# Performance work log

Measured on AMD Instinct MI355X. Metric: run time of the kernel, lower is better.

## Reference

```python
import jax, jax.numpy as jnp
import numpy as np

B, N, F, H, F_ = 2048, 8192, 512, 8, 64

def setup_inputs() -> dict:
    key = jax.random.key(0)
    k1, k2, k3, k4 = jax.random.split(key, 4)
    X = jax.random.normal(k1, (B, F), dtype=jnp.float32)
    G = jax.random.normal(k2, (N, F), dtype=jnp.float32)
    W = jax.random.normal(k3, (H, F, F_), dtype=jnp.float32) * 0.05   # per-head kernels
    att = jax.random.normal(k4, (H, 2 * F_), dtype=jnp.float32) * 0.05  # per-head att kernels (2F_,1) flattened
    return {"X": X, "G": G, "W": W, "att": att}

def reference(X, G, W, att):
    f_ = W.shape[-1]
    # Per-head linear transforms
    WhX = jnp.einsum('bf,hfe->hbe', X, W)   # [H,B,F_]
    WhG = jnp.einsum('nf,hfe->hne', G, W)   # [H,N,F_]
    # concat([WhX_i, WhG_j]) @ a  ==  WhX_i @ a1 + WhG_j @ a2  -> avoids tiled [B*N,2F_]
    a1, a2 = att[:, :f_], att[:, f_:]
    e1 = jnp.einsum('hbe,he->hb', WhX, a1)  # [H,B]
    e2 = jnp.einsum('hne,he->hn', WhG, a2)  # [H,N]
    scores = e1[:, :, None] + e2[:, None, :]            # [H,B,N] pairwise logits
    attn = jax.nn.softmax(scores, axis=-1)              # softmax over graph nodes
    out = jnp.einsum('hbn,hne->hbe', attn, WhG)         # weighted aggregate [H,B,F_]
    out = jax.nn.relu(out)                              # concat-mode applies activation per head
    # concat heads -> [B, H*F_]
    return jnp.transpose(out, (1, 0, 2)).reshape(out.shape[1], -1)
```

## Files before the change

kernel.cpp:

```cpp
#include <hip/hip_runtime.h>


#define HF   8
#define FDIM 512
#define FE   64
#define NG   8192
#define BX   2048
#define NBLK 128
#define NTHR 512
#define ROWSPB (NG / NBLK)

#define WS_W2   64
#define WS_SP   4224
#define WS_PART 8192

__global__ __launch_bounds__(256) void k_init(const float* __restrict__ W,
                                              const float* __restrict__ att,
                                              float* __restrict__ ws) {
    int bid = blockIdx.x, tid = threadIdx.x;
    if (bid == 0 && tid == 0)
        __hip_atomic_store(reinterpret_cast<unsigned int*>(ws), 0u,
                           __ATOMIC_RELAXED, __HIP_MEMORY_SCOPE_AGENT);

    int o = bid * 64 + (tid >> 2);
    int sub = tid & 3;
    int h = o >> 9;
    const float* wp = W + (size_t)o * FE + sub * 16;
    const float* a2 = att + h * (2 * FE) + FE + sub * 16;
    float s = 0.f;
#pragma unroll
    for (int e = 0; e < 16; e += 4) {
        float4 w4 = *reinterpret_cast<const float4*>(wp + e);
        s += w4.x * a2[e] + w4.y * a2[e + 1] + w4.z * a2[e + 2] + w4.w * a2[e + 3];
    }
    s += __shfl_xor(s, 1, 64);
    s += __shfl_xor(s, 2, 64);
    if (sub == 0) ws[WS_W2 + o] = s;
}

__global__ __launch_bounds__(NTHR, 1) void k_fused(const float* __restrict__ G,
                                                   const float* __restrict__ W,
                                                   float* __restrict__ ws,
                                                   float* __restrict__ out) {
    __shared__ float lds2[2][HF * FDIM];
    __shared__ float s_lds[8][HF];
    __shared__ float gh[FDIM];
    __shared__ float vp[32][17];
    __shared__ float vrs[16];
    __shared__ float s_tmp[128];
    __shared__ float s_red[8];
    __shared__ float s_h_lds;

    int bid = blockIdx.x, tid = threadIdx.x;
    int wave = tid >> 6, lane = tid & 63;
    const float* w2g = ws + WS_W2;
    float* s_part = ws + WS_SP;
    float* part   = ws + WS_PART;
    unsigned int* counter = reinterpret_cast<unsigned int*>(ws);

    float4 w2a[HF], w2b[HF];
#pragma unroll
    for (int h = 0; h < HF; ++h) {
        const float* wp = w2g + h * FDIM + lane * 8;
        w2a[h] = *reinterpret_cast<const float4*>(wp);
        w2b[h] = *reinterpret_cast<const float4*>(wp + 4);
    }
    float4 accA[HF], accB[HF];
#pragma unroll
    for (int h = 0; h < HF; ++h) {
        accA[h] = make_float4(0.f, 0.f, 0.f, 0.f);
        accB[h] = make_float4(0.f, 0.f, 0.f, 0.f);
    }
    float s_acc[HF] = {};

    int n0 = bid * ROWSPB + wave * (ROWSPB / 8);
    for (int r = 0; r < ROWSPB / 8; ++r) {
        const float* gp = G + (size_t)(n0 + r) * FDIM + lane * 8;
        float4 g0 = *reinterpret_cast<const float4*>(gp);
        float4 g1 = *reinterpret_cast<const float4*>(gp + 4);
        float e[HF];
#pragma unroll
        for (int h = 0; h < HF; ++h)
            e[h] = g0.x * w2a[h].x + g0.y * w2a[h].y + g0.z * w2a[h].z + g0.w * w2a[h].w
                 + g1.x * w2b[h].x + g1.y * w2b[h].y + g1.z * w2b[h].z + g1.w * w2b[h].w;
#pragma unroll
        for (int off = 32; off > 0; off >>= 1) {
#pragma unroll
            for (int h = 0; h < HF; ++h) e[h] += __shfl_xor(e[h], off, 64);
        }
#pragma unroll
        for (int h = 0; h < HF; ++h) {
            float w = __expf(e[h]);
            s_acc[h] += w;
            accA[h].x = fmaf(w, g0.x, accA[h].x);
            accA[h].y = fmaf(w, g0.y, accA[h].y);
            accA[h].z = fmaf(w, g0.z, accA[h].z);
            accA[h].w = fmaf(w, g0.w, accA[h].w);
            accB[h].x = fmaf(w, g1.x, accB[h].x);
            accB[h].y = fmaf(w, g1.y, accB[h].y);
            accB[h].z = fmaf(w, g1.z, accB[h].z);
            accB[h].w = fmaf(w, g1.w, accB[h].w);
        }
    }

    if (lane == 0) {
#pragma unroll
        for (int h = 0; h < HF; ++h) s_lds[wave][h] = s_acc[h];
    }

    for (int rnd = 0; rnd < 4; ++rnd) {
        if ((wave >> 1) == rnd) {
            int buf = wave & 1;
#pragma unroll
            for (int h = 0; h < HF; ++h) {
                float* dst = lds2[buf] + h * FDIM + lane * 8;
                if (rnd == 0) {
                    *reinterpret_cast<float4*>(dst)     = accA[h];
                    *reinterpret_cast<float4*>(dst + 4) = accB[h];
                } else {
                    float4 t0 = *reinterpret_cast<float4*>(dst);
                    float4 t1 = *reinterpret_cast<float4*>(dst + 4);
                    t0.x += accA[h].x; t0.y += accA[h].y; t0.z += accA[h].z; t0.w += accA[h].w;
                    t1.x += accB[h].x; t1.y += accB[h].y; t1.z += accB[h].z; t1.w += accB[h].w;
                    *reinterpret_cast<float4*>(dst)     = t0;
                    *reinterpret_cast<float4*>(dst + 4) = t1;
                }
            }
        }
        __syncthreads();
    }

    {
        float* pdst = part + (size_t)bid * (HF * FDIM);
        for (int i = tid; i < HF * FDIM; i += NTHR)
            __hip_atomic_store(&pdst[i], lds2[0][i] + lds2[1][i],
                               __ATOMIC_RELAXED, __HIP_MEMORY_SCOPE_AGENT);
        if (tid < HF) {
            float sv = 0.f;
#pragma unroll
            for (int w = 0; w < 8; ++w) sv += s_lds[w][tid];
            __hip_atomic_store(&s_part[bid * HF + tid], sv,
                               __ATOMIC_RELAXED, __HIP_MEMORY_SCOPE_AGENT);
        }
    }

    __syncthreads();
    if (tid == 0) {
        __hip_atomic_fetch_add(counter, 1u, __ATOMIC_RELAXED, __HIP_MEMORY_SCOPE_AGENT);
        int iters = 0;
        while (__hip_atomic_load(counter, __ATOMIC_RELAXED, __HIP_MEMORY_SCOPE_AGENT) < NBLK) {
            __builtin_amdgcn_s_sleep(2);
            if (++iters > 400000) break;
        }
    }
    __syncthreads();

    int slice = bid & 31, rc = bid >> 5;
    int h = slice >> 2, e0 = (slice & 3) * 16;

    {
        float acc = 0.f;
        const float* pcol = part + (h << 9) + tid;
#pragma unroll 8
        for (int p = 0; p < NBLK; ++p)
            acc += __hip_atomic_load(pcol + (size_t)p * (HF * FDIM),
                                     __ATOMIC_RELAXED, __HIP_MEMORY_SCOPE_AGENT);
        gh[tid] = acc;
    }
    if (tid < 128)
        s_tmp[tid] = __hip_atomic_load(&s_part[tid * HF + h],
                                       __ATOMIC_RELAXED, __HIP_MEMORY_SCOPE_AGENT);
    __syncthreads();
    if (tid < 8) {
        float v = 0.f;
#pragma unroll
        for (int k = 0; k < 16; ++k) v += s_tmp[tid * 16 + k];
        s_red[tid] = v;
    }
    __syncthreads();
    if (tid == 0) {
        float v = 0.f;
#pragma unroll
        for (int k = 0; k < 8; ++k) v += s_red[k];
        s_h_lds = v;
    }
    __syncthreads();

    {
        int e = tid & 15, fg = tid >> 4;
        const float* wp = W + (size_t)h * FDIM * FE + (size_t)(fg * 16) * FE + e0 + e;
        float a = 0.f;
#pragma unroll
        for (int k = 0; k < 16; ++k)
            a = fmaf(gh[fg * 16 + k], wp[(size_t)k * FE], a);
        vp[fg][e] = a;
    }
    __syncthreads();
    if (tid < 16) {
        float v = 0.f;
#pragma unroll
        for (int j = 0; j < 32; ++j) v += vp[j][tid];
        vrs[tid] = fmaxf(v / s_h_lds, 0.f);
    }
    __syncthreads();

    {
        int row = rc * 512 + tid;
        float4* dst = reinterpret_cast<float4*>(out + (size_t)row * FDIM + h * FE + e0);
        dst[0] = make_float4(vrs[0],  vrs[1],  vrs[2],  vrs[3]);
        dst[1] = make_float4(vrs[4],  vrs[5],  vrs[6],  vrs[7]);
        dst[2] = make_float4(vrs[8],  vrs[9],  vrs[10], vrs[11]);
        dst[3] = make_float4(vrs[12], vrs[13], vrs[14], vrs[15]);
    }
}

extern "C" void kernel_launch(void* const* d_in, const int* in_sizes, int n_in,
                              void* d_out, int out_size, void* d_ws, size_t ws_size,
                              hipStream_t stream) {
    const float* G   = (const float*)d_in[1];
    const float* W   = (const float*)d_in[2];
    const float* att = (const float*)d_in[3];
    float* out = (float*)d_out;
    float* ws  = (float*)d_ws;

    k_init <<<64,   256,  0, stream>>>(W, att, ws);
    k_fused<<<NBLK, NTHR, 0, stream>>>(G, W, ws, out);
}
```

Measured before the change: 43.53 us.

## Split fused kernel into separate pass kernels, replacing spin-wait grid barrier

Replaces the atomic-counter grid barrier inside the fused kernel with a kernel boundary. The G pass and the final reduction/projection now run as separate launches. Partial stores and loads become plain vectorized float4 accesses instead of relaxed atomics, and the cross-block reduction is split across four thread groups. The w2 precompute kernel is retiled to use more blocks with one float4 per thread. This removes spin-wait polling and scalar atomic traffic at the cost of one extra kernel launch.

```diff
diff --git a/kernel.cpp b/kernel.cpp
--- a/kernel.cpp
+++ b/kernel.cpp
@@ -10,53 +10,35 @@
 #define NTHR 512
 #define ROWSPB (NG / NBLK)
 
-#define WS_W2   64
-#define WS_SP   4224
+#define WS_SP   4096
 #define WS_PART 8192
 
-__global__ __launch_bounds__(256) void k_init(const float* __restrict__ W,
-                                              const float* __restrict__ att,
-                                              float* __restrict__ ws) {
-    int bid = blockIdx.x, tid = threadIdx.x;
-    if (bid == 0 && tid == 0)
-        __hip_atomic_store(reinterpret_cast<unsigned int*>(ws), 0u,
-                           __ATOMIC_RELAXED, __HIP_MEMORY_SCOPE_AGENT);
-
-    int o = bid * 64 + (tid >> 2);
-    int sub = tid & 3;
+__global__ __launch_bounds__(256) void k_w2(const float* __restrict__ W,
+                                            const float* __restrict__ att,
+                                            float* __restrict__ w2) {
+    int o = blockIdx.x * 16 + (threadIdx.x >> 4);
+    int sub = threadIdx.x & 15;
     int h = o >> 9;
-    const float* wp = W + (size_t)o * FE + sub * 16;
-    const float* a2 = att + h * (2 * FE) + FE + sub * 16;
-    float s = 0.f;
-#pragma unroll
-    for (int e = 0; e < 16; e += 4) {
-        float4 w4 = *reinterpret_cast<const float4*>(wp + e);
-        s += w4.x * a2[e] + w4.y * a2[e + 1] + w4.z * a2[e + 2] + w4.w * a2[e + 3];
-    }
+    float4 w4 = *reinterpret_cast<const float4*>(W + (size_t)o * FE + sub * 4);
+    const float* a2 = att + h * (2 * FE) + FE + sub * 4;
+    float s = w4.x * a2[0] + w4.y * a2[1] + w4.z * a2[2] + w4.w * a2[3];
     s += __shfl_xor(s, 1, 64);
     s += __shfl_xor(s, 2, 64);
-    if (sub == 0) ws[WS_W2 + o] = s;
-}
-
-__global__ __launch_bounds__(NTHR, 1) void k_fused(const float* __restrict__ G,
-                                                   const float* __restrict__ W,
-                                                   float* __restrict__ ws,
-                                                   float* __restrict__ out) {
+    s += __shfl_xor(s, 4, 64);
+    s += __shfl_xor(s, 8, 64);
+    if (sub == 0) w2[o] = s;
+}
+
+__global__ __launch_bounds__(NTHR, 1) void k_gpass(const float* __restrict__ G,
+                                                   const float* __restrict__ w2g,
+                                                   float* __restrict__ ws) {
     __shared__ float lds2[2][HF * FDIM];
     __shared__ float s_lds[8][HF];
-    __shared__ float gh[FDIM];
-    __shared__ float vp[32][17];
-    __shared__ float vrs[16];
-    __shared__ float s_tmp[128];
-    __shared__ float s_red[8];
-    __shared__ float s_h_lds;
 
     int bid = blockIdx.x, tid = threadIdx.x;
     int wave = tid >> 6, lane = tid & 63;
-    const float* w2g = ws + WS_W2;
     float* s_part = ws + WS_SP;
     float* part   = ws + WS_PART;
-    unsigned int* counter = reinterpret_cast<unsigned int*>(ws);
 
     float4 w2a[HF], w2b[HF];
 #pragma unroll
@@ -131,57 +113,63 @@
     }
 
     {
-        float* pdst = part + (size_t)bid * (HF * FDIM);
-        for (int i = tid; i < HF * FDIM; i += NTHR)
-            __hip_atomic_store(&pdst[i], lds2[0][i] + lds2[1][i],
-                               __ATOMIC_RELAXED, __HIP_MEMORY_SCOPE_AGENT);
+        float4* pdst = reinterpret_cast<float4*>(part + (size_t)bid * (HF * FDIM));
+        const float4* a = reinterpret_cast<const float4*>(lds2[0]);
+        const float4* b = reinterpret_cast<const float4*>(lds2[1]);
+        for (int i = tid; i < HF * FDIM / 4; i += NTHR) {
+            float4 x = a[i], y = b[i];
+            x.x += y.x; x.y += y.y; x.z += y.z; x.w += y.w;
+            pdst[i] = x;
+        }
         if (tid < HF) {
             float sv = 0.f;
 #pragma unroll
             for (int w = 0; w < 8; ++w) sv += s_lds[w][tid];
-            __hip_atomic_store(&s_part[bid * HF + tid], sv,
-                               __ATOMIC_RELAXED, __HIP_MEMORY_SCOPE_AGENT);
-        }
-    }
-
-    __syncthreads();
-    if (tid == 0) {
-        __hip_atomic_fetch_add(counter, 1u, __ATOMIC_RELAXED, __HIP_MEMORY_SCOPE_AGENT);
-        int iters = 0;
-        while (__hip_atomic_load(counter, __ATOMIC_RELAXED, __HIP_MEMORY_SCOPE_AGENT) < NBLK) {
-            __builtin_amdgcn_s_sleep(2);
-            if (++iters > 400000) break;
-        }
-    }
-    __syncthreads();
+            s_part[bid * HF + tid] = sv;
+        }
+    }
+}
+
+__global__ __launch_bounds__(NTHR, 1) void k_vr(const float* __restrict__ W,
+                                                const float* __restrict__ ws,
+                                                float* __restrict__ out) {
+    __shared__ float4 red4[4][128];
+    __shared__ float gh[FDIM];
+    __shared__ float vp[32][17];
+    __shared__ float vrs[16];
+    __shared__ float s_tmp[128];
+    __shared__ float s_h_lds;
+
+    int bid = blockIdx.x, tid = threadIdx.x;
+    const float* s_part = ws + WS_SP;
+    const float* part   = ws + WS_PART;
 
     int slice = bid & 31, rc = bid >> 5;
     int h = slice >> 2, e0 = (slice & 3) * 16;
 
     {
-        float acc = 0.f;
-        const float* pcol = part + (h << 9) + tid;
+        int fq = tid & 127, pg = tid >> 7;
+        const float4* pcol = reinterpret_cast<const float4*>(part + (size_t)h * FDIM) + fq;
+        float4 a = make_float4(0.f, 0.f, 0.f, 0.f);
 #pragma unroll 8
-        for (int p = 0; p < NBLK; ++p)
-            acc += __hip_atomic_load(pcol + (size_t)p * (HF * FDIM),
-                                     __ATOMIC_RELAXED, __HIP_MEMORY_SCOPE_AGENT);
-        gh[tid] = acc;
-    }
-    if (tid < 128)
-        s_tmp[tid] = __hip_atomic_load(&s_part[tid * HF + h],
-                                       __ATOMIC_RELAXED, __HIP_MEMORY_SCOPE_AGENT);
-    __syncthreads();
-    if (tid < 8) {
-        float v = 0.f;
-#pragma unroll
-        for (int k = 0; k < 16; ++k) v += s_tmp[tid * 16 + k];
-        s_red[tid] = v;
-    }
-    __syncthreads();
+        for (int p = 0; p < 32; ++p) {
+            float4 v = pcol[(size_t)(pg * 32 + p) * (HF * FDIM / 4)];
+            a.x += v.x; a.y += v.y; a.z += v.z; a.w += v.w;
+        }
+        red4[pg][fq] = a;
+    }
+    if (tid >= 256 && tid < 384)
+        s_tmp[tid - 256] = s_part[(tid - 256) * HF + h];
+    __syncthreads();
+    if (tid < 128) {
+        float4 a = red4[0][tid], b = red4[1][tid], c = red4[2][tid], d = red4[3][tid];
+        float4 r = make_float4((a.x + b.x) + (c.x + d.x), (a.y + b.y) + (c.y + d.y),
+                               (a.z + b.z) + (c.z + d.z), (a.w + b.w) + (c.w + d.w));
+        reinterpret_cast<float4*>(gh)[tid] = r;
+    }
     if (tid == 0) {
         float v = 0.f;
-#pragma unroll
-        for (int k = 0; k < 8; ++k) v += s_red[k];
+        for (int k = 0; k < 128; ++k) v += s_tmp[k];
         s_h_lds = v;
     }
     __syncthreads();
@@ -223,6 +211,7 @@
     float* out = (float*)d_out;
     float* ws  = (float*)d_ws;
 
-    k_init <<<64,   256,  0, stream>>>(W, att, ws);
-    k_fused<<<NBLK, NTHR, 0, stream>>>(G, W, ws, out);
-}
+    k_w2   <<<256,  256,  0, stream>>>(W, att, ws);
+    k_gpass<<<NBLK, NTHR, 0, stream>>>(G, ws, ws);
+    k_vr   <<<NBLK, NTHR, 0, stream>>>(W, ws, out);
+}
```

After: 39.56 us. 9.1% less time.
